# Optimization experiments

Hardware: AMD Instinct MI355X
Metric: run time of the kernel (lower is better)

Reference implementation:

```python
import jax, jax.numpy as jnp
import numpy as np

H = 1024  # hidden_size
I = 256   # input_size
C = 1000  # num_classes


def _lstm_layer(x, Wih, Whh, b):
    """Single LSTM layer, batch_first x: [B,T,Din] -> [B,T,H].
    PyTorch gate order: i, f, g, o."""
    B = x.shape[0]
    Hh = Whh.shape[1]
    # precompute input-to-hidden projections for all timesteps
    xg = jnp.einsum('btd,gd->btg', x, Wih) + b  # [B,T,4H]
    xg = jnp.swapaxes(xg, 0, 1)  # [T,B,4H]

    def step(carry, xg_t):
        h, c = carry
        g = xg_t + h @ Whh.T  # [B,4H]
        i, f, gg, o = jnp.split(g, 4, axis=-1)
        i = jax.nn.sigmoid(i)
        f = jax.nn.sigmoid(f)
        gg = jnp.tanh(gg)
        o = jax.nn.sigmoid(o)
        c = f * c + i * gg
        h = o * jnp.tanh(c)
        return (h, c), h

    h0 = jnp.zeros((B, Hh), dtype=x.dtype)
    c0 = jnp.zeros((B, Hh), dtype=x.dtype)
    (_, _), hs = jax.lax.scan(step, (h0, c0), xg)
    return jnp.swapaxes(hs, 0, 1)  # [B,T,H]


def setup_inputs() -> dict:
    key = jax.random.key(0)
    ks = jax.random.split(key, 12)
    s = 1.0 / np.sqrt(H)
    u = lambda k, shp: jax.random.uniform(k, shp, jnp.float32, -s, s)
    x = jax.random.normal(ks[0], (64, 512, I), dtype=jnp.float32)
    return {
        'x': x,
        'Wih0': u(ks[1], (4 * H, I)),
        'Whh0': u(ks[2], (4 * H, H)),
        'b0': u(ks[3], (4 * H,)) + u(ks[4], (4 * H,)),  # b_ih + b_hh
        'Wih1': u(ks[5], (4 * H, H)),
        'Whh1': u(ks[6], (4 * H, H)),
        'b1': u(ks[7], (4 * H,)) + u(ks[8], (4 * H,)),
        'Wfc': u(ks[9], (C, H)),
        'bfc': u(ks[10], (C,)),
    }


def reference(x, Wih0, Whh0, b0, Wih1, Whh1, b1, Wfc, bfc):
    h1 = _lstm_layer(x, Wih0, Whh0, b0)    # [B,T,H]
    h2 = _lstm_layer(h1, Wih1, Whh1, b1)   # [B,T,H]
    out = h2[:, -1, :] @ Wfc.T + bfc       # [B,C]
    return jax.nn.relu(out)
```

## Files before the change

### kernel.cpp

```cpp
#include <hip/hip_runtime.h>
#include <cmath>

typedef _Float16 f16x8 __attribute__((ext_vector_type(8)));
typedef float f32x4 __attribute__((ext_vector_type(4)));

namespace {

constexpr int kB = 64;
constexpr int kT = 512;
constexpr int kI = 256;
constexpr int kH = 1024;
constexpr int kNC = 1000;
constexpr int kKc = 128;
constexpr int kLP = kKc + 8;

__device__ __forceinline__ float sigmoidf_(float x) {
  return 1.0f / (1.0f + expf(-x));
}

__device__ __forceinline__ f16x8 ldh8(const _Float16* p) {
  return *reinterpret_cast<const f16x8*>(p);
}

__device__ __forceinline__ float dot4_(float4 a, float4 b) {
  return a.x * b.x + a.y * b.y + a.z * b.z + a.w * b.w;
}

__device__ void lstm_phase_mfma(
    int tid, int u0, int nChunks, int len0,
    const _Float16* __restrict__ Whi, const _Float16* __restrict__ Wlo,
    const _Float16* __restrict__ in0h, const _Float16* __restrict__ in0l,
    const _Float16* __restrict__ in1h, const _Float16* __restrict__ in1l,
    const float* __restrict__ bias, float* __restrict__ c_st,
    _Float16* __restrict__ houth, _Float16* __restrict__ houtl,
    float* __restrict__ houtf,
    _Float16 (*Ahi)[kLP], _Float16 (*Alo)[kLP]) {
  const int lane = tid & 63;
  const int wave = tid >> 6;
  const int K = nChunks * kKc;

  const int sr = tid >> 4;
  const int sk = (tid & 15) * 8;
  const int grow = (sr & 3) * kH + u0 + (sr >> 2);
  const _Float16* wsrc_h = Whi + (size_t)grow * K + sk;
  const _Float16* wsrc_l = Wlo + (size_t)grow * K + sk;

  const int kg = (lane >> 4) * 8;
  const int am = lane & 15;
  const int b = wave * 16 + (lane & 15);

  f32x4 acc = {0.f, 0.f, 0.f, 0.f};

  f16x8 wrh = ldh8(wsrc_h);
  f16x8 wrl = ldh8(wsrc_l);
  f16x8 bh[4], bl[4];
#pragma unroll
  for (int ks = 0; ks < 4; ++ks) {
    const int gk = ks * 32 + kg;
    const _Float16* ph;
    const _Float16* pl;
    if (gk < len0) {
      ph = in0h + (size_t)b * len0 + gk;
      pl = in0l + (size_t)b * len0 + gk;
    } else {
      ph = in1h + (size_t)b * kH + (gk - len0);
      pl = in1l + (size_t)b * kH + (gk - len0);
    }
    bh[ks] = ldh8(ph);
    bl[ks] = ldh8(pl);
  }

  for (int c = 0; c < nChunks; ++c) {
    __syncthreads();
    *reinterpret_cast<f16x8*>(&Ahi[sr][sk]) = wrh;
    *reinterpret_cast<f16x8*>(&Alo[sr][sk]) = wrl;
    if (c + 1 < nChunks) {
      wrh = ldh8(wsrc_h + (size_t)(c + 1) * kKc);
      wrl = ldh8(wsrc_l + (size_t)(c + 1) * kKc);
    }
    __syncthreads();
    f16x8 nbh[4], nbl[4];
    if (c + 1 < nChunks) {
      const int k0n = (c + 1) * kKc;
#pragma unroll
      for (int ks = 0; ks < 4; ++ks) {
        const int gk = k0n + ks * 32 + kg;
        const _Float16* ph;
        const _Float16* pl;
        if (gk < len0) {
          ph = in0h + (size_t)b * len0 + gk;
          pl = in0l + (size_t)b * len0 + gk;
        } else {
          ph = in1h + (size_t)b * kH + (gk - len0);
          pl = in1l + (size_t)b * kH + (gk - len0);
        }
        nbh[ks] = ldh8(ph);
        nbl[ks] = ldh8(pl);
      }
    }
#pragma unroll
    for (int ks = 0; ks < 4; ++ks) {
      const int kk = ks * 32 + kg;
      f16x8 ah = ldh8(&Ahi[am][kk]);
      f16x8 al = ldh8(&Alo[am][kk]);
      acc = __builtin_amdgcn_mfma_f32_16x16x32_f16(ah, bh[ks], acc, 0, 0, 0);
      acc = __builtin_amdgcn_mfma_f32_16x16x32_f16(ah, bl[ks], acc, 0, 0, 0);
      acc = __builtin_amdgcn_mfma_f32_16x16x32_f16(al, bh[ks], acc, 0, 0, 0);
    }
#pragma unroll
    for (int ks = 0; ks < 4; ++ks) {
      bh[ks] = nbh[ks];
      bl[ks] = nbl[ks];
    }
  }

  const int eb = wave * 16 + (lane & 15);
  const int eu = u0 + (lane >> 4);
  const size_t idx = (size_t)eb * kH + eu;
  const float gi = sigmoidf_(acc[0] + bias[eu]);
  const float gf = sigmoidf_(acc[1] + bias[kH + eu]);
  const float gg = tanhf(acc[2] + bias[2 * kH + eu]);
  const float go = sigmoidf_(acc[3] + bias[3 * kH + eu]);
  const float cn = gf * c_st[idx] + gi * gg;
  c_st[idx] = cn;
  const float h = go * tanhf(cn);
  const _Float16 hh = (_Float16)h;
  houth[idx] = hh;
  houtl[idx] = (_Float16)(h - (float)hh);
  if (houtf) houtf[idx] = h;
}

__global__ __launch_bounds__(256) void lstm_step(
    int s,
    const _Float16* __restrict__ WAh, const _Float16* __restrict__ WAl,
    const _Float16* __restrict__ WBh, const _Float16* __restrict__ WBl,
    const _Float16* __restrict__ XSh, const _Float16* __restrict__ XSl,
    _Float16* __restrict__ hA, _Float16* __restrict__ hB,
    const float* __restrict__ b0v, const float* __restrict__ b1v,
    float* __restrict__ cA, float* __restrict__ cB,
    float* __restrict__ h2f) {
  __shared__ _Float16 Ahi[16][kLP];
  __shared__ _Float16 Alo[16][kLP];
  const int tid = threadIdx.x;
  const int u0 = blockIdx.x * 4;
  const int HS = kB * kH;
  const int pPrev = (s + 1) & 1, pCur = s & 1;

  _Float16* hAprevH = hA + (size_t)pPrev * 2 * HS;
  _Float16* hAprevL = hAprevH + HS;
  _Float16* hAcurH = hA + (size_t)pCur * 2 * HS;
  _Float16* hAcurL = hAcurH + HS;
  _Float16* hBprevH = hB + (size_t)pCur * 2 * HS;
  _Float16* hBprevL = hBprevH + HS;
  _Float16* hBcurH = hB + (size_t)pPrev * 2 * HS;
  _Float16* hBcurL = hBcurH + HS;

  if (s < kT) {
    lstm_phase_mfma(tid, u0, (kI + kH) / kKc, kI, WAh, WAl,
                    XSh + (size_t)s * kB * kI, XSl + (size_t)s * kB * kI,
                    hAprevH, hAprevL, b0v, cA, hAcurH, hAcurL, nullptr, Ahi,
                    Alo);
  }
  __syncthreads();
  if (s >= 1) {
    lstm_phase_mfma(tid, u0, (kH + kH) / kKc, kH, WBh, WBl, hAprevH, hAprevL,
                    hBprevH, hBprevL, b1v, cB, hBcurH, hBcurL, h2f, Ahi, Alo);
  }
}

__global__ __launch_bounds__(256) void prep_wsplit(
    const float* __restrict__ W0, int k0len, const float* __restrict__ W1,
    int k1len, _Float16* __restrict__ oh, _Float16* __restrict__ ol,
    int total) {
  const int K = k0len + k1len;
  for (int i = blockIdx.x * blockDim.x + threadIdx.x; i < total;
       i += gridDim.x * blockDim.x) {
    const int row = i / K, k = i % K;
    const float v = (k < k0len) ? W0[(size_t)row * k0len + k]
                                : W1[(size_t)row * k1len + (k - k0len)];
    const _Float16 h = (_Float16)v;
    oh[i] = h;
    ol[i] = (_Float16)(v - (float)h);
  }
}

__global__ __launch_bounds__(256) void prep_xsplit(
    const float* __restrict__ x, _Float16* __restrict__ oh,
    _Float16* __restrict__ ol) {
  const int total = kT * kB * kI;
  for (int i = blockIdx.x * blockDim.x + threadIdx.x; i < total;
       i += gridDim.x * blockDim.x) {
    const int k = i % kI;
    const int rem = i / kI;
    const int bb = rem % kB;
    const int t = rem / kB;
    const float v = x[((size_t)bb * kT + t) * kI + k];
    const _Float16 h = (_Float16)v;
    oh[i] = h;
    ol[i] = (_Float16)(v - (float)h);
  }
}

__global__ __launch_bounds__(256) void fc_kernel(
    const float* __restrict__ h, const float* __restrict__ Wfc,
    const float* __restrict__ bfc, float* __restrict__ out) {
  __shared__ float in_lds[kB][132];
  const int tid = threadIdx.x;
  const int cls = blockIdx.x * 4 + (tid & 3);
  const int b = tid >> 2;
  float acc = bfc[cls];
  for (int c = 0; c < kH / 128; ++c) {
    {
      const int sb = tid >> 2, sc = tid & 3;
#pragma unroll
      for (int j = 0; j < 8; ++j) {
        const int kk = (sc + j * 4) * 4;
        *reinterpret_cast<float4*>(&in_lds[sb][kk]) =
            *reinterpret_cast<const float4*>(h + (size_t)sb * kH + c * 128 + kk);
      }
    }
    __syncthreads();
    const float* wrow = Wfc + (size_t)cls * kH + c * 128;
#pragma unroll
    for (int k = 0; k < 128; k += 4) {
      float4 w = *reinterpret_cast<const float4*>(wrow + k);
      float4 v = *reinterpret_cast<const float4*>(&in_lds[b][k]);
      acc += dot4_(w, v);
    }
    __syncthreads();
  }
  out[(size_t)b * kNC + cls] = fmaxf(acc, 0.0f);
}

}

extern "C" void kernel_launch(void* const* d_in, const int* in_sizes, int n_in,
                              void* d_out, int out_size, void* d_ws, size_t ws_size,
                              hipStream_t stream) {
  const float* x    = (const float*)d_in[0];
  const float* Wih0 = (const float*)d_in[1];
  const float* Whh0 = (const float*)d_in[2];
  const float* b0   = (const float*)d_in[3];
  const float* Wih1 = (const float*)d_in[4];
  const float* Whh1 = (const float*)d_in[5];
  const float* b1   = (const float*)d_in[6];
  const float* Wfc  = (const float*)d_in[7];
  const float* bfc  = (const float*)d_in[8];
  float* out = (float*)d_out;

  char* w = (char*)d_ws;
  size_t off = 0;
  auto a16 = [&](size_t n) {
    _Float16* p = (_Float16*)(w + off);
    off += n * sizeof(_Float16);
    return p;
  };
  const size_t HS = (size_t)kB * kH;
  _Float16* WAh = a16((size_t)4 * kH * (kI + kH));
  _Float16* WAl = a16((size_t)4 * kH * (kI + kH));
  _Float16* WBh = a16((size_t)4 * kH * (2 * kH));
  _Float16* WBl = a16((size_t)4 * kH * (2 * kH));
  _Float16* XSh = a16((size_t)kT * kB * kI);
  _Float16* XSl = a16((size_t)kT * kB * kI);
  _Float16* hA  = a16(4 * HS);
  _Float16* hB  = a16(4 * HS);
  float* cA = (float*)(w + off); off += HS * sizeof(float);
  float* cB = (float*)(w + off); off += HS * sizeof(float);
  float* h2f = (float*)(w + off); off += HS * sizeof(float);

  hipMemsetAsync(hA, 0, 8 * HS * sizeof(_Float16) + 2 * HS * sizeof(float),
                 stream);

  prep_wsplit<<<1024, 256, 0, stream>>>(Wih0, kI, Whh0, kH, WAh, WAl,
                                        4 * kH * (kI + kH));
  prep_wsplit<<<1024, 256, 0, stream>>>(Wih1, kH, Whh1, kH, WBh, WBl,
                                        4 * kH * (2 * kH));
  prep_xsplit<<<1024, 256, 0, stream>>>(x, XSh, XSl);

  for (int s = 0; s <= kT; ++s) {
    lstm_step<<<256, 256, 0, stream>>>(s, WAh, WAl, WBh, WBl, XSh, XSl, hA, hB,
                                       b0, b1, cA, cB, h2f);
  }
  fc_kernel<<<kNC / 4, 256, 0, stream>>>(h2f, Wfc, bfc, out);
}
```

Baseline: 17.61 ms.

## Split K across two wave groups per block with LDS reduction in LSTM step

Doubles the block to 512 threads and splits the reduction dimension into two halves, each handled by four waves with its own LDS weight tile. The partial accumulators are combined through a shared float4 buffer before the gate nonlinearities. The weight prefetch is also deepened to two chunks ahead. This shortens the serial K loop per step to cut per-timestep latency, in exchange for an extra barrier, more LDS, and half the threads sitting idle during the epilogue.

```diff
diff --git a/kernel.cpp b/kernel.cpp
--- a/kernel.cpp
+++ b/kernel.cpp
@@ -27,38 +27,38 @@
 }
 
 __device__ void lstm_phase_mfma(
-    int tid, int u0, int nChunks, int len0,
+    int tid, int u0, int Khalf, int len0,
     const _Float16* __restrict__ Whi, const _Float16* __restrict__ Wlo,
     const _Float16* __restrict__ in0h, const _Float16* __restrict__ in0l,
     const _Float16* __restrict__ in1h, const _Float16* __restrict__ in1l,
     const float* __restrict__ bias, float* __restrict__ c_st,
     _Float16* __restrict__ houth, _Float16* __restrict__ houtl,
     float* __restrict__ houtf,
-    _Float16 (*Ahi)[kLP], _Float16 (*Alo)[kLP]) {
+    _Float16 (*Ahi)[16][kLP], _Float16 (*Alo)[16][kLP],
+    float4 (*red)[64]) {
   const int lane = tid & 63;
   const int wave = tid >> 6;
-  const int K = nChunks * kKc;
-
-  const int sr = tid >> 4;
-  const int sk = (tid & 15) * 8;
+  const int kh = wave >> 2;
+  const int nw = wave & 3;
+  const int K = 2 * Khalf;
+  const int kbase0 = kh * Khalf;
+  const int nC = Khalf / kKc;
+
+  const int st = tid & 255;
+  const int sr = st >> 4;
+  const int sk = (st & 15) * 8;
+  const int sgh = tid >> 8;
   const int grow = (sr & 3) * kH + u0 + (sr >> 2);
-  const _Float16* wsrc_h = Whi + (size_t)grow * K + sk;
-  const _Float16* wsrc_l = Wlo + (size_t)grow * K + sk;
+  const _Float16* wsrc_h = Whi + (size_t)grow * K + (size_t)sgh * Khalf + sk;
+  const _Float16* wsrc_l = Wlo + (size_t)grow * K + (size_t)sgh * Khalf + sk;
 
   const int kg = (lane >> 4) * 8;
   const int am = lane & 15;
-  const int b = wave * 16 + (lane & 15);
+  const int b = nw * 16 + (lane & 15);
 
   f32x4 acc = {0.f, 0.f, 0.f, 0.f};
 
-  f16x8 wrh = ldh8(wsrc_h);
-  f16x8 wrl = ldh8(wsrc_l);
-  f16x8 bh[4], bl[4];
-#pragma unroll
-  for (int ks = 0; ks < 4; ++ks) {
-    const int gk = ks * 32 + kg;
-    const _Float16* ph;
-    const _Float16* pl;
+  auto baddr = [&](int gk, const _Float16*& ph, const _Float16*& pl) {
     if (gk < len0) {
       ph = in0h + (size_t)b * len0 + gk;
       pl = in0l + (size_t)b * len0 + gk;
@@ -66,71 +66,80 @@
       ph = in1h + (size_t)b * kH + (gk - len0);
       pl = in1l + (size_t)b * kH + (gk - len0);
     }
-    bh[ks] = ldh8(ph);
-    bl[ks] = ldh8(pl);
-  }
-
-  for (int c = 0; c < nChunks; ++c) {
-    __syncthreads();
-    *reinterpret_cast<f16x8*>(&Ahi[sr][sk]) = wrh;
-    *reinterpret_cast<f16x8*>(&Alo[sr][sk]) = wrl;
-    if (c + 1 < nChunks) {
-      wrh = ldh8(wsrc_h + (size_t)(c + 1) * kKc);
-      wrl = ldh8(wsrc_l + (size_t)(c + 1) * kKc);
-    }
+  };
+
+  f16x8 wh0 = ldh8(wsrc_h);
+  f16x8 wl0 = ldh8(wsrc_l);
+  f16x8 wh1 = ldh8(wsrc_h + kKc);
+  f16x8 wl1 = ldh8(wsrc_l + kKc);
+
+  f16x8 bhv[4], blv[4];
+#pragma unroll
+  for (int ks = 0; ks < 4; ++ks) {
+    const _Float16 *ph, *pl;
+    baddr(kbase0 + ks * 32 + kg, ph, pl);
+    bhv[ks] = ldh8(ph);
+    blv[ks] = ldh8(pl);
+  }
+
+  for (int c = 0; c < nC; ++c) {
+    __syncthreads();
+    *reinterpret_cast<f16x8*>(&Ahi[sgh][sr][sk]) = wh0;
+    *reinterpret_cast<f16x8*>(&Alo[sgh][sr][sk]) = wl0;
+    wh0 = wh1;
+    wl0 = wl1;
+    const int cw = (c + 2 < nC) ? (c + 2) : (nC - 1);
+    wh1 = ldh8(wsrc_h + (size_t)cw * kKc);
+    wl1 = ldh8(wsrc_l + (size_t)cw * kKc);
     __syncthreads();
     f16x8 nbh[4], nbl[4];
-    if (c + 1 < nChunks) {
-      const int k0n = (c + 1) * kKc;
-#pragma unroll
-      for (int ks = 0; ks < 4; ++ks) {
-        const int gk = k0n + ks * 32 + kg;
-        const _Float16* ph;
-        const _Float16* pl;
-        if (gk < len0) {
-          ph = in0h + (size_t)b * len0 + gk;
-          pl = in0l + (size_t)b * len0 + gk;
-        } else {
-          ph = in1h + (size_t)b * kH + (gk - len0);
-          pl = in1l + (size_t)b * kH + (gk - len0);
-        }
-        nbh[ks] = ldh8(ph);
-        nbl[ks] = ldh8(pl);
-      }
-    }
+    const int cb = (c + 1 < nC) ? (c + 1) : (nC - 1);
 #pragma unroll
     for (int ks = 0; ks < 4; ++ks) {
-      const int kk = ks * 32 + kg;
-      f16x8 ah = ldh8(&Ahi[am][kk]);
-      f16x8 al = ldh8(&Alo[am][kk]);
-      acc = __builtin_amdgcn_mfma_f32_16x16x32_f16(ah, bh[ks], acc, 0, 0, 0);
-      acc = __builtin_amdgcn_mfma_f32_16x16x32_f16(ah, bl[ks], acc, 0, 0, 0);
-      acc = __builtin_amdgcn_mfma_f32_16x16x32_f16(al, bh[ks], acc, 0, 0, 0);
+      const _Float16 *ph, *pl;
+      baddr(kbase0 + cb * kKc + ks * 32 + kg, ph, pl);
+      nbh[ks] = ldh8(ph);
+      nbl[ks] = ldh8(pl);
     }
 #pragma unroll
     for (int ks = 0; ks < 4; ++ks) {
-      bh[ks] = nbh[ks];
-      bl[ks] = nbl[ks];
-    }
-  }
-
-  const int eb = wave * 16 + (lane & 15);
-  const int eu = u0 + (lane >> 4);
-  const size_t idx = (size_t)eb * kH + eu;
-  const float gi = sigmoidf_(acc[0] + bias[eu]);
-  const float gf = sigmoidf_(acc[1] + bias[kH + eu]);
-  const float gg = tanhf(acc[2] + bias[2 * kH + eu]);
-  const float go = sigmoidf_(acc[3] + bias[3 * kH + eu]);
-  const float cn = gf * c_st[idx] + gi * gg;
-  c_st[idx] = cn;
-  const float h = go * tanhf(cn);
-  const _Float16 hh = (_Float16)h;
-  houth[idx] = hh;
-  houtl[idx] = (_Float16)(h - (float)hh);
-  if (houtf) houtf[idx] = h;
-}
-
-__global__ __launch_bounds__(256) void lstm_step(
+      f16x8 ah = ldh8(&Ahi[kh][am][ks * 32 + kg]);
+      f16x8 al = ldh8(&Alo[kh][am][ks * 32 + kg]);
+      acc = __builtin_amdgcn_mfma_f32_16x16x32_f16(ah, bhv[ks], acc, 0, 0, 0);
+      acc = __builtin_amdgcn_mfma_f32_16x16x32_f16(ah, blv[ks], acc, 0, 0, 0);
+      acc = __builtin_amdgcn_mfma_f32_16x16x32_f16(al, bhv[ks], acc, 0, 0, 0);
+    }
+#pragma unroll
+    for (int ks = 0; ks < 4; ++ks) {
+      bhv[ks] = nbh[ks];
+      blv[ks] = nbl[ks];
+    }
+  }
+
+  if (kh == 1) {
+    red[nw][lane] = make_float4(acc[0], acc[1], acc[2], acc[3]);
+  }
+  __syncthreads();
+  if (kh == 0) {
+    const float4 p = red[nw][lane];
+    const int eb = nw * 16 + (lane & 15);
+    const int eu = u0 + (lane >> 4);
+    const size_t idx = (size_t)eb * kH + eu;
+    const float gi = sigmoidf_(acc[0] + p.x + bias[eu]);
+    const float gf = sigmoidf_(acc[1] + p.y + bias[kH + eu]);
+    const float gg = tanhf(acc[2] + p.z + bias[2 * kH + eu]);
+    const float go = sigmoidf_(acc[3] + p.w + bias[3 * kH + eu]);
+    const float cn = gf * c_st[idx] + gi * gg;
+    c_st[idx] = cn;
+    const float h = go * tanhf(cn);
+    const _Float16 hh = (_Float16)h;
+    houth[idx] = hh;
+    houtl[idx] = (_Float16)(h - (float)hh);
+    if (houtf) houtf[idx] = h;
+  }
+}
+
+__global__ __launch_bounds__(512, 2) void lstm_step(
     int s,
     const _Float16* __restrict__ WAh, const _Float16* __restrict__ WAl,
     const _Float16* __restrict__ WBh, const _Float16* __restrict__ WBl,
@@ -139,8 +148,9 @@
     const float* __restrict__ b0v, const float* __restrict__ b1v,
     float* __restrict__ cA, float* __restrict__ cB,
     float* __restrict__ h2f) {
-  __shared__ _Float16 Ahi[16][kLP];
-  __shared__ _Float16 Alo[16][kLP];
+  __shared__ _Float16 Ahi[2][16][kLP];
+  __shared__ _Float16 Alo[2][16][kLP];
+  __shared__ float4 red[4][64];
   const int tid = threadIdx.x;
   const int u0 = blockIdx.x * 4;
   const int HS = kB * kH;
@@ -156,15 +166,15 @@
   _Float16* hBcurL = hBcurH + HS;
 
   if (s < kT) {
-    lstm_phase_mfma(tid, u0, (kI + kH) / kKc, kI, WAh, WAl,
+    lstm_phase_mfma(tid, u0, (kI + kH) / 2, kI, WAh, WAl,
                     XSh + (size_t)s * kB * kI, XSl + (size_t)s * kB * kI,
                     hAprevH, hAprevL, b0v, cA, hAcurH, hAcurL, nullptr, Ahi,
-                    Alo);
+                    Alo, red);
   }
   __syncthreads();
   if (s >= 1) {
-    lstm_phase_mfma(tid, u0, (kH + kH) / kKc, kH, WBh, WBl, hAprevH, hAprevL,
-                    hBprevH, hBprevL, b1v, cB, hBcurH, hBcurL, h2f, Ahi, Alo);
+    lstm_phase_mfma(tid, u0, kH, kH, WBh, WBl, hAprevH, hAprevL, hBprevH,
+                    hBprevL, b1v, cB, hBcurH, hBcurL, h2f, Ahi, Alo, red);
   }
 }
 
@@ -278,7 +288,7 @@
   prep_xsplit<<<1024, 256, 0, stream>>>(x, XSh, XSl);
 
   for (int s = 0; s <= kT; ++s) {
-    lstm_step<<<256, 256, 0, stream>>>(s, WAh, WAl, WBh, WBl, XSh, XSl, hA, hB,
+    lstm_step<<<256, 512, 0, stream>>>(s, WAh, WAl, WBh, WBl, XSh, XSl, hA, hB,
                                        b0, b1, cA, cB, h2f);
   }
   fc_kernel<<<kNC / 4, 256, 0, stream>>>(h2f, Wfc, bfc, out);
```

Result: faster. 15.91 ms (-9.6%).
